# Kernel tuning notes

Hardware: AMD Instinct MI355X
Metric: run time of the kernel (lower is better)

Reference implementation:

```python
import jax, jax.numpy as jnp
import numpy as np

B, N, E, T, S = 4096, 16, 512, 128, 256  # batch, num_experts, expert_dim, task_dim, scenario_dim


def setup_inputs() -> dict:
    key = jax.random.key(0)
    k1, k2, k3, k4 = jax.random.split(key, 4)
    return {
        "scene_repr": jax.random.normal(k1, (B, S), dtype=jnp.float32),
        "task_anchor": jax.random.normal(k2, (B, T), dtype=jnp.float32),
        "expert_reprs": jax.random.normal(k3, (B, N, E), dtype=jnp.float32),
        "v": jax.random.normal(k4, (E + T, 1), dtype=jnp.float32),
    }


def reference(scene_repr, task_anchor, expert_reprs, v):
    # Original: score_i = concat([expert_i, task_anchor]) @ v for each expert i.
    # Vectorized: split v into expert part and task part; task contribution is
    # identical for every expert, so compute it once and broadcast.
    E_ = expert_reprs.shape[-1]
    v_e = v[:E_, 0]   # [E]
    v_t = v[E_:, 0]   # [T]
    scores = jnp.einsum('bne,e->bn', expert_reprs, v_e) + (task_anchor @ v_t)[:, None]  # [B, N]
    attention_weights = jax.nn.softmax(scores, axis=1)  # [B, N]
    aggregated_repr = jnp.einsum('bne,bn->be', expert_reprs, attention_weights)  # [B, E]
    return aggregated_repr, attention_weights
```

## Files before the change

### kernel.cpp

```cpp
#include <hip/hip_runtime.h>


#define NB 4096
#define NEXP 16
#define EDIM 512

typedef float f32x2 __attribute__((ext_vector_type(2)));

__global__ __launch_bounds__(256, 4) void meta_attn_kernel(
    const float* __restrict__ expert,
    const float* __restrict__ v,
    float* __restrict__ out_agg,
    float* __restrict__ out_w)
{
    const int wave = threadIdx.x >> 6;
    const int lane = threadIdx.x & 63;
    const int b = blockIdx.x;

    __shared__ float smem[NEXP * EDIM];
    __shared__ float lds_s[NEXP][4];

    {
        const float* gbase = expert + (size_t)b * (NEXP * EDIM) + wave * 2048;
        float* lbase = smem + wave * 2048;
#pragma unroll
        for (int i = 0; i < 8; ++i) {
            __builtin_amdgcn_global_load_lds(
                (const __attribute__((address_space(1))) void*)(gbase + i * 256 + lane * 4),
                (__attribute__((address_space(3))) void*)(lbase + i * 256),
                16, 0, 0);
        }
    }

    const int eoff = 128 * wave + 2 * lane;
    const f32x2 ve = *(const f32x2*)(v + eoff);

    __syncthreads();

    float cur[NEXP];
#pragma unroll
    for (int n = 0; n < NEXP; ++n) {
        const f32x2 t = *(const f32x2*)(&smem[n * EDIM + eoff]);
        cur[n] = t.x * ve.x + t.y * ve.y;
    }

    float t8[8];
    {
        const bool hi = (lane & 1) != 0;
#pragma unroll
        for (int j = 0; j < 8; ++j) {
            const float send = hi ? cur[j] : cur[j + 8];
            const float keep = hi ? cur[j + 8] : cur[j];
            t8[j] = keep + __shfl_xor(send, 1, 64);
        }
    }
    float t4[4];
    {
        const bool hi = (lane & 2) != 0;
#pragma unroll
        for (int j = 0; j < 4; ++j) {
            const float send = hi ? t8[j] : t8[j + 4];
            const float keep = hi ? t8[j + 4] : t8[j];
            t4[j] = keep + __shfl_xor(send, 2, 64);
        }
    }
    float t2[2];
    {
        const bool hi = (lane & 4) != 0;
#pragma unroll
        for (int j = 0; j < 2; ++j) {
            const float send = hi ? t4[j] : t4[j + 2];
            const float keep = hi ? t4[j + 2] : t4[j];
            t2[j] = keep + __shfl_xor(send, 4, 64);
        }
    }
    float t1;
    {
        const bool hi = (lane & 8) != 0;
        const float send = hi ? t2[0] : t2[1];
        const float keep = hi ? t2[1] : t2[0];
        t1 = keep + __shfl_xor(send, 8, 64);
    }
    t1 += __shfl_xor(t1, 16, 64);
    t1 += __shfl_xor(t1, 32, 64);

    if (lane < 16) {
        const int idx = ((lane & 1) << 3) | ((lane & 2) << 1) |
                        ((lane & 4) >> 1) | ((lane & 8) >> 3);
        lds_s[idx][wave] = t1;
    }
    __syncthreads();

    float s[NEXP];
#pragma unroll
    for (int n = 0; n < NEXP; ++n)
        s[n] = (lds_s[n][0] + lds_s[n][1]) + (lds_s[n][2] + lds_s[n][3]);

    float mx = s[0];
#pragma unroll
    for (int n = 1; n < NEXP; ++n) mx = fmaxf(mx, s[n]);
    float w[NEXP];
    float sum = 0.0f;
#pragma unroll
    for (int n = 0; n < NEXP; ++n) {
        w[n] = __expf(s[n] - mx);
        sum += w[n];
    }
    const float inv = 1.0f / sum;
#pragma unroll
    for (int n = 0; n < NEXP; ++n) w[n] *= inv;

    f32x2 acc = {0.f, 0.f};
#pragma unroll
    for (int n = 0; n < NEXP; ++n) {
        const f32x2 t = *(const f32x2*)(&smem[n * EDIM + eoff]);
        acc.x += w[n] * t.x;
        acc.y += w[n] * t.y;
    }
    *(f32x2*)(out_agg + (size_t)b * EDIM + eoff) = acc;

    if (wave == 0) {
        float myw = w[0];
#pragma unroll
        for (int n = 1; n < NEXP; ++n) myw = (lane == n) ? w[n] : myw;
        if (lane < NEXP) out_w[(size_t)b * NEXP + lane] = myw;
    }
}

extern "C" void kernel_launch(void* const* d_in, const int* in_sizes, int n_in,
                              void* d_out, int out_size, void* d_ws, size_t ws_size,
                              hipStream_t stream) {
    const float* expert = (const float*)d_in[2];
    const float* v      = (const float*)d_in[3];
    float* out_agg = (float*)d_out;
    float* out_w   = (float*)d_out + (size_t)NB * EDIM;

    meta_attn_kernel<<<dim3(NB), dim3(256), 0, stream>>>(expert, v, out_agg, out_w);
}
```

Measured before the change: 27.38 us.

## Stage expert tiles in registers and double-buffer four batch rows per block

The 32KB shared-memory staging via global_load_lds is replaced with direct per-thread register loads of the expert tile. Each block now handles four batch rows, loading the next row's tile into a second register buffer while the current one is processed. The grid shrinks fourfold, and the __syncthreads calls become lighter explicit waitcnt plus s_barrier pairs. Freeing LDS should raise occupancy and overlap loads with compute, at the cost of fewer blocks, more registers per thread and extra barriers per row.

```diff
diff --git a/kernel.cpp b/kernel.cpp
--- a/kernel.cpp
+++ b/kernel.cpp
@@ -4,45 +4,28 @@
 #define NB 4096
 #define NEXP 16
 #define EDIM 512
+#define BPB 4
 
 typedef float f32x2 __attribute__((ext_vector_type(2)));
 
-__global__ __launch_bounds__(256, 4) void meta_attn_kernel(
-    const float* __restrict__ expert,
-    const float* __restrict__ v,
-    float* __restrict__ out_agg,
-    float* __restrict__ out_w)
-{
-    const int wave = threadIdx.x >> 6;
-    const int lane = threadIdx.x & 63;
-    const int b = blockIdx.x;
+__device__ __forceinline__ void load_tile(f32x2 (&T)[NEXP],
+                                          const float* __restrict__ expert,
+                                          int b, int eoff) {
+    const float* row = expert + (size_t)b * (NEXP * EDIM) + eoff;
+#pragma unroll
+    for (int n = 0; n < NEXP; ++n)
+        T[n] = *(const f32x2*)(row + n * EDIM);
+}
 
-    __shared__ float smem[NEXP * EDIM];
-    __shared__ float lds_s[NEXP][4];
-
-    {
-        const float* gbase = expert + (size_t)b * (NEXP * EDIM) + wave * 2048;
-        float* lbase = smem + wave * 2048;
-#pragma unroll
-        for (int i = 0; i < 8; ++i) {
-            __builtin_amdgcn_global_load_lds(
-                (const __attribute__((address_space(1))) void*)(gbase + i * 256 + lane * 4),
-                (__attribute__((address_space(3))) void*)(lbase + i * 256),
-                16, 0, 0);
-        }
-    }
-
-    const int eoff = 128 * wave + 2 * lane;
-    const f32x2 ve = *(const f32x2*)(v + eoff);
-
-    __syncthreads();
-
+__device__ __forceinline__ void process_b(const f32x2 (&T)[NEXP], f32x2 ve,
+                                          int wave, int lane, int b, int eoff,
+                                          float (*lds_s)[4],
+                                          float* __restrict__ out_agg,
+                                          float* __restrict__ out_w) {
     float cur[NEXP];
 #pragma unroll
-    for (int n = 0; n < NEXP; ++n) {
-        const f32x2 t = *(const f32x2*)(&smem[n * EDIM + eoff]);
-        cur[n] = t.x * ve.x + t.y * ve.y;
-    }
+    for (int n = 0; n < NEXP; ++n)
+        cur[n] = T[n].x * ve.x + T[n].y * ve.y;
 
     float t8[8];
     {
@@ -89,7 +72,9 @@
                         ((lane & 4) >> 1) | ((lane & 8) >> 3);
         lds_s[idx][wave] = t1;
     }
-    __syncthreads();
+    asm volatile("s_waitcnt lgkmcnt(0)" ::: "memory");
+    __builtin_amdgcn_s_barrier();
+    asm volatile("" ::: "memory");
 
     float s[NEXP];
 #pragma unroll
@@ -113,9 +98,8 @@
     f32x2 acc = {0.f, 0.f};
 #pragma unroll
     for (int n = 0; n < NEXP; ++n) {
-        const f32x2 t = *(const f32x2*)(&smem[n * EDIM + eoff]);
-        acc.x += w[n] * t.x;
-        acc.y += w[n] * t.y;
+        acc.x += w[n] * T[n].x;
+        acc.y += w[n] * T[n].y;
     }
     *(f32x2*)(out_agg + (size_t)b * EDIM + eoff) = acc;
 
@@ -125,6 +109,37 @@
         for (int n = 1; n < NEXP; ++n) myw = (lane == n) ? w[n] : myw;
         if (lane < NEXP) out_w[(size_t)b * NEXP + lane] = myw;
     }
+
+    asm volatile("s_waitcnt lgkmcnt(0)" ::: "memory");
+    __builtin_amdgcn_s_barrier();
+    asm volatile("" ::: "memory");
+}
+
+__global__ __launch_bounds__(256, 4) void meta_attn_kernel(
+    const float* __restrict__ expert,
+    const float* __restrict__ v,
+    float* __restrict__ out_agg,
+    float* __restrict__ out_w)
+{
+    const int wave = threadIdx.x >> 6;
+    const int lane = threadIdx.x & 63;
+    const int b0 = blockIdx.x * BPB;
+    const int eoff = 128 * wave + 2 * lane;
+
+    __shared__ float lds_s[NEXP][4];
+
+    const f32x2 ve = *(const f32x2*)(v + eoff);
+
+    f32x2 TA[NEXP], TB[NEXP];
+
+    load_tile(TA, expert, b0 + 0, eoff);
+    load_tile(TB, expert, b0 + 1, eoff);
+    process_b(TA, ve, wave, lane, b0 + 0, eoff, lds_s, out_agg, out_w);
+    load_tile(TA, expert, b0 + 2, eoff);
+    process_b(TB, ve, wave, lane, b0 + 1, eoff, lds_s, out_agg, out_w);
+    load_tile(TB, expert, b0 + 3, eoff);
+    process_b(TA, ve, wave, lane, b0 + 2, eoff, lds_s, out_agg, out_w);
+    process_b(TB, ve, wave, lane, b0 + 3, eoff, lds_s, out_agg, out_w);
 }
 
 extern "C" void kernel_launch(void* const* d_in, const int* in_sizes, int n_in,
@@ -135,5 +150,5 @@
     float* out_agg = (float*)d_out;
     float* out_w   = (float*)d_out + (size_t)NB * EDIM;
 
-    meta_attn_kernel<<<dim3(NB), dim3(256), 0, stream>>>(expert, v, out_agg, out_w);
+    meta_attn_kernel<<<dim3(NB / BPB), dim3(256), 0, stream>>>(expert, v, out_agg, out_w);
 }
```

Result: slower. 29.04 us (+6.1%).
